# Kernel tuning notes

Measured on AMD Instinct MI355X. Metric: run time of the kernel, lower is better.

## Reference

```python
import jax, jax.numpy as jnp
import numpy as np

B, T, DIM = 1, 2048, 1024
NUM_HEADS, HEAD_DIM = 8, 128
ATTN_SCALE = 0.12


def _rms_norm(x):
    # F.rms_norm(x, x.size(-1)) with no weight; eps defaults to machine eps
    eps = jnp.asarray(jnp.finfo(x.dtype).eps, x.dtype)
    return x * jax.lax.rsqrt(jnp.mean(x * x, axis=-1, keepdims=True) + eps)


def _rotary_tables(seq_len, head_dim):
    # (1/1024) ** linspace(0,1,head_dim//4), then pad with head_dim//4 zeros
    freq = (1.0 / 1024.0) ** jnp.linspace(0.0, 1.0, head_dim // 4, dtype=jnp.float32)
    ang = jnp.concatenate([freq, jnp.zeros(head_dim // 4, jnp.float32)])  # [hd/2]
    theta = jnp.arange(seq_len, dtype=jnp.float32)[:, None] * ang[None, :]  # [T, hd/2]
    return jnp.cos(theta), jnp.sin(theta)


def _apply_rotary(x, cos, sin):
    # x: [B, T, H, hd]
    x1, x2 = jnp.split(x.astype(jnp.float32), 2, axis=-1)
    c = cos[None, :, None, :]
    s = sin[None, :, None, :]
    y1 = x1 * c + x2 * s
    y2 = -x1 * s + x2 * c
    return jnp.concatenate([y1, y2], axis=-1).astype(x.dtype)


def setup_inputs() -> dict:
    key = jax.random.key(0)
    ks = jax.random.split(key, 5)
    bound = (3.0 ** 0.5) * 0.5 * DIM ** (-0.5)
    x = jax.random.normal(ks[0], (B, T, DIM), jnp.float32)
    ve = jax.random.normal(ks[1], (B, T, NUM_HEADS * HEAD_DIM), jnp.float32)
    qkv_w = jax.random.uniform(ks[2], (3, NUM_HEADS * HEAD_DIM, DIM), jnp.float32, -bound, bound)
    lambdas = jnp.array([0.5, 0.5], jnp.float32)
    # original zero-inits c_proj; use small random weight so the output is nontrivial
    c_proj_w = jax.random.uniform(ks[3], (DIM, NUM_HEADS * HEAD_DIM), jnp.float32, -bound, bound)
    return {"x": x, "ve": ve, "qkv_w": qkv_w, "lambdas": lambdas, "c_proj_w": c_proj_w}


def reference(x, ve, qkv_w, lambdas, c_proj_w):
    Bx, Tx, D = x.shape
    H, hd = NUM_HEADS, HEAD_DIM
    # fused QKV projection: weight [3*H*hd, D]
    qkv = x @ qkv_w.reshape(3 * H * hd, D).T            # [B, T, 3*H*hd]
    qkv = qkv.reshape(Bx, Tx, 3 * H, hd)
    q, k, v = jnp.split(qkv, 3, axis=-2)                # each [B, T, H, hd]
    q, k = _rms_norm(q), _rms_norm(k)
    cos, sin = _rotary_tables(Tx, hd)
    q, k = _apply_rotary(q, cos, sin), _apply_rotary(k, cos, sin)
    v = lambdas[0] * v + lambdas[1] * ve.reshape(v.shape)
    att = jnp.einsum('bthd,bshd->bhts', q, k) * ATTN_SCALE
    causal = jnp.tril(jnp.ones((Tx, Tx), bool))
    att = jnp.where(causal[None, None], att, -jnp.inf)
    att = jax.nn.softmax(att, axis=-1)
    y = jnp.einsum('bhts,bshd->bthd', att, v).reshape(Bx, Tx, H * hd)
    return y @ c_proj_w.T
```

## Files before the change

### kernel.cpp

```cpp
#include <hip/hip_runtime.h>


typedef __attribute__((ext_vector_type(8))) short short8;
typedef __attribute__((ext_vector_type(4))) short short4b;
typedef __attribute__((ext_vector_type(4))) float fx4;
typedef __attribute__((ext_vector_type(8))) unsigned short ushort8;
typedef __attribute__((ext_vector_type(4))) unsigned short ushort4v;
typedef __attribute__((ext_vector_type(2))) unsigned short ushort2v;
typedef __attribute__((ext_vector_type(4))) float float4v;

#define T_SEQ 2048
#define NH 8
#define HD 128

__device__ __forceinline__ unsigned short f2bf(float f) {
  union { float f; unsigned u; } v; v.f = f;
  unsigned u = v.u;
  u += 0x7fffu + ((u >> 16) & 1u);
  return (unsigned short)(u >> 16);
}
__device__ __forceinline__ short bf_t(float f) {
  union { float f; unsigned u; } v; v.f = f;
  return (short)(v.u >> 16);
}
__device__ __forceinline__ float bf2f(unsigned short h) {
  union { unsigned u; float f; } v; v.u = ((unsigned)h) << 16;
  return v.f;
}

typedef __attribute__((address_space(1))) unsigned int glb_u32;
typedef __attribute__((address_space(3))) unsigned int lds_u32;
__device__ __forceinline__ void gl_lds16(const unsigned short* g, unsigned short* l) {
  __builtin_amdgcn_global_load_lds((const glb_u32*)g, (lds_u32*)l, 16, 0, 0);
}

__global__ __launch_bounds__(256) void cast3_kernel(
    const float* __restrict__ x, const float* __restrict__ w1,
    const float* __restrict__ w2, unsigned short* __restrict__ o) {
  long q = (long)blockIdx.x * 256 + threadIdx.x;
  const float* src;
  if (q < 524288)        src = x  + 4 * q;
  else if (q < 1310720)  src = w1 + 4 * (q - 524288);
  else                   src = w2 + 4 * (q - 1310720);
  float4v v = *(const float4v*)src;
  ushort4v r;
  r[0] = f2bf(v[0]); r[1] = f2bf(v[1]); r[2] = f2bf(v[2]); r[3] = f2bf(v[3]);
  *(ushort4v*)(o + 4 * q) = r;
}

template <bool OUT_BF16, int BM, int BN, int BK>
__global__ __launch_bounds__(256) void gemm_bt5(
    const unsigned short* __restrict__ A, const unsigned short* __restrict__ B,
    void* __restrict__ Cp, int M, int N, int K) {
  constexpr int MT = BM / 32;
  constexpr int NT = BN / 32;
  constexpr int KQ = BK / 32;
  constexpr int CPR = BK / 8;
  constexpr int ASEG = BM * BK / 512;
  constexpr int NLOAD = (BM + BN) * BK / 512 / 4;
  __shared__ unsigned short a_sh[2][BM * BK];
  __shared__ unsigned short b_sh[2][BN * BK];
  const int tid = threadIdx.x;
  const int wave = tid >> 6, lane = tid & 63;
  const int ln = lane & 15, quad = lane >> 4;
  const int wm = wave & 1, wn = wave >> 1;
  const long arow0 = (long)blockIdx.y * BM;
  const long brow0 = (long)blockIdx.x * BN;

  const unsigned short* gsrc[NLOAD];
  unsigned short* ldst[NLOAD];
  int bstr[NLOAD];
  for (int i = 0; i < NLOAD; ++i) {
    int s = wave * NLOAD + i;
    int isB = s >= ASEG;
    int srel = isB ? s - ASEG : s;
    int li = srel * 64 + lane;
    int row = li / CPR, posc = li % CPR;
    int c = posc ^ ((row >> 1) & (CPR - 1));
    gsrc[i] = (isB ? B + brow0 * (long)K : A + arow0 * (long)K)
              + (long)row * K + c * 8;
    ldst[i] = (isB ? &b_sh[0][0] : &a_sh[0][0]) + srel * 512;
    bstr[i] = (isB ? BN : BM) * BK;
  }
  for (int i = 0; i < NLOAD; ++i) gl_lds16(gsrc[i], ldst[i]);

  fx4 acc[MT][NT] = {};
  int cur = 0;
  for (int k0 = 0; k0 < K; k0 += BK, cur ^= 1) {
    __syncthreads();
    if (k0 + BK < K)
      for (int i = 0; i < NLOAD; ++i)
        gl_lds16(gsrc[i] + k0 + BK, ldst[i] + (cur ^ 1) * bstr[i]);
    const unsigned short* ash = &a_sh[cur][0];
    const unsigned short* bsh = &b_sh[cur][0];
    short8 af[KQ][MT], bfr[KQ][NT];
    for (int kq = 0; kq < KQ; ++kq) {
      for (int mt = 0; mt < MT; ++mt) {
        int m = wm * (BM / 2) + mt * 16 + ln;
        int pos = (kq * 4 + quad) ^ ((m >> 1) & (CPR - 1));
        af[kq][mt] = *(const short8*)&ash[m * BK + pos * 8];
      }
      for (int nt = 0; nt < NT; ++nt) {
        int n = wn * (BN / 2) + nt * 16 + ln;
        int pos = (kq * 4 + quad) ^ ((n >> 1) & (CPR - 1));
        bfr[kq][nt] = *(const short8*)&bsh[n * BK + pos * 8];
      }
    }
    for (int kq = 0; kq < KQ; ++kq)
      for (int mt = 0; mt < MT; ++mt)
        for (int nt = 0; nt < NT; ++nt)
          acc[mt][nt] = __builtin_amdgcn_mfma_f32_16x16x32_bf16(
              af[kq][mt], bfr[kq][nt], acc[mt][nt], 0, 0, 0);
  }
  for (int mt = 0; mt < MT; ++mt)
    for (int nt = 0; nt < NT; ++nt)
      for (int r = 0; r < 4; ++r) {
        long row = arow0 + wm * (BM / 2) + mt * 16 + quad * 4 + r;
        long col = brow0 + wn * (BN / 2) + nt * 16 + ln;
        float v = acc[mt][nt][r];
        if constexpr (OUT_BF16)
          ((unsigned short*)Cp)[row * N + col] = f2bf(v);
        else
          ((float*)Cp)[row * N + col] = v;
      }
}

__global__ __launch_bounds__(256) void qk_norm_rope2(
    const unsigned short* __restrict__ qkv, unsigned short* __restrict__ qh,
    unsigned short* __restrict__ kh) {
  const int idx = blockIdx.x * 4 + (threadIdx.x >> 6);
  const int lane = threadIdx.x & 63;
  const int which = idx & 1, h = (idx >> 1) & 7, t = idx >> 4;
  const unsigned short* src = qkv + (long)t * 3072 + which * 1024 + h * 128;
  float x1 = bf2f(src[lane]);
  float x2 = bf2f(src[64 + lane]);
  float ss = x1 * x1 + x2 * x2;
  for (int off = 1; off < 64; off <<= 1) ss += __shfl_xor(ss, off);
  float rn = rsqrtf(ss * (1.0f / 128.0f) + 1.1920929e-7f);
  float ang = (lane < 32) ? exp2f(-10.0f * (float)lane / 31.0f) : 0.0f;
  float th = (float)t * ang;
  float sv = __sinf(th), cv = __cosf(th);
  float y1 = ( x1 * cv + x2 * sv) * rn;
  float y2 = (-x1 * sv + x2 * cv) * rn;
  unsigned short* dst = (which ? kh : qh) + ((long)h * T_SEQ + t) * 128;
  dst[lane] = f2bf(y1);
  dst[64 + lane] = f2bf(y2);
}

__global__ __launch_bounds__(256) void v_combine_t(
    const unsigned short* __restrict__ qkv, const float* __restrict__ ve,
    const float* __restrict__ lambdas, unsigned short* __restrict__ vt) {
  __shared__ unsigned short lt[128 * 72];
  const int tt = blockIdx.x, h = blockIdx.y;
  const int tid = threadIdx.x;
  const float l0 = lambdas[0], l1 = lambdas[1];
  const int r = tid >> 2, cb = (tid & 3) * 32;
  const unsigned short* vs = qkv + (long)(tt * 64 + r) * 3072 + 2048 + h * 128 + cb;
  const float* es = ve + (long)(tt * 64 + r) * 1024 + h * 128 + cb;
  ushort8 vv[4];
  for (int q = 0; q < 4; ++q) vv[q] = *(const ushort8*)(vs + 8 * q);
  float4v ee[8];
  for (int q = 0; q < 8; ++q) ee[q] = *(const float4v*)(es + 4 * q);
  for (int j = 0; j < 32; ++j) {
    float v = bf2f(vv[j >> 3][j & 7]) * l0 + ee[j >> 2][j & 3] * l1;
    lt[(cb + j) * 72 + r] = f2bf(v);
  }
  __syncthreads();
  const int d = tid >> 1, half = tid & 1;
  unsigned short* dst = vt + ((long)h * HD + d) * T_SEQ + tt * 64 + half * 32;
  const unsigned short* srcl = &lt[d * 72];
  for (int g = 0; g < 8; ++g) {
    int p0 = half * 32 + g * 4;
    int kv0 = ((p0 >> 5) & 1) * 32 + ((p0 >> 2) & 1) * 16 + ((p0 >> 3) & 3) * 4;
    *(ushort4v*)(dst + g * 4) = *(const ushort4v*)(srcl + kv0);
  }
}

#define ATT_C1 0.17312340490667562f
#define ATT_C2 23.083120654223415f

__global__ __launch_bounds__(256, 2) void attn_part(
    const unsigned short* __restrict__ qh, const unsigned short* __restrict__ kh,
    const unsigned short* __restrict__ vt, unsigned short* __restrict__ Yp,
    float* __restrict__ lp) {
  __shared__ unsigned short kbuf[2][8192];
  __shared__ unsigned short vbuf[2][8192];
  const int tid = threadIdx.x;
  const int wave = tid >> 6, lane = tid & 63;
  const int ln = lane & 15, quad = lane >> 4;
  const int qt = blockIdx.x, h = blockIdx.y, ch = blockIdx.z;
  const int jmax = 2 * qt + 1;
  const int j0 = ch * 4;
  if (j0 > jmax) return;
  const int j1 = min(j0 + 3, jmax);

  int qg[2];
  short8 qf[2][4];
  for (int s = 0; s < 2; ++s) {
    qg[s] = qt * 128 + wave * 32 + s * 16 + ln;
    const unsigned short* qbase = qh + ((long)h * T_SEQ + qg[s]) * 128;
    for (int kc = 0; kc < 4; ++kc)
      qf[s][kc] = *(const short8*)(qbase + kc * 32 + quad * 8);
  }
  fx4 accy[2][8] = {};
  float l_loc[2] = {0.f, 0.f};

  const unsigned short* kg[4]; unsigned short* kl[4];
  const unsigned short* vg[4]; unsigned short* vl[4];
  for (int i = 0; i < 4; ++i) {
    int s = wave * 4 + i;
    { int li = s * 64 + lane; int row = li >> 4, posc = li & 15;
      int c = posc ^ (row & 15);
      kg[i] = kh + ((long)h * T_SEQ + row) * 128 + c * 8;
      kl[i] = &kbuf[0][s * 512]; }
    { int li = s * 64 + lane; int row = li >> 3, posc = li & 7;
      int c = posc ^ (row & 7);
      vg[i] = vt + ((long)h * HD + row) * T_SEQ + c * 8;
      vl[i] = &vbuf[0][s * 512]; }
  }
  for (int i = 0; i < 4; ++i) gl_lds16(kg[i] + (long)j0 * 8192, kl[i]);
  for (int i = 0; i < 4; ++i) gl_lds16(vg[i] + (long)j0 * 64, vl[i]);

  int cur = 0;
  for (int jt = j0; jt <= j1; ++jt, cur ^= 1) {
    __syncthreads();
    if (jt < j1) {
      int nb = (cur ^ 1) * 8192;
      for (int i = 0; i < 4; ++i) gl_lds16(kg[i] + (long)(jt + 1) * 8192, kl[i] + nb);
      for (int i = 0; i < 4; ++i) gl_lds16(vg[i] + (long)(jt + 1) * 64, vl[i] + nb);
    }
    const unsigned short* kb_ = &kbuf[cur][0];
    fx4 s4[2][4];
    for (int kt = 0; kt < 4; ++kt) {
      s4[0][kt] = fx4{0.f, 0.f, 0.f, 0.f};
      s4[1][kt] = fx4{0.f, 0.f, 0.f, 0.f};
      for (int kc = 0; kc < 4; ++kc) {
        int pos = (kc * 4 + quad) ^ ln;
        short8 kf = *(const short8*)&kb_[(kt * 16 + ln) * 128 + pos * 8];
        s4[0][kt] = __builtin_amdgcn_mfma_f32_16x16x32_bf16(kf, qf[0][kc], s4[0][kt], 0, 0, 0);
        s4[1][kt] = __builtin_amdgcn_mfma_f32_16x16x32_bf16(kf, qf[1][kc], s4[1][kt], 0, 0, 0);
      }
    }
    short4b pb[2][4];
    for (int s = 0; s < 2; ++s)
      for (int kt = 0; kt < 4; ++kt) {
        int kvb = jt * 64 + kt * 16 + quad * 4;
        float p[4];
        for (int r = 0; r < 4; ++r)
          p[r] = exp2f(fmaf(s4[s][kt][r], ATT_C1, -ATT_C2));
        if (jt * 64 + kt * 16 + 15 > qt * 128 + wave * 32 + s * 16) {
          for (int r = 0; r < 4; ++r) if (kvb + r > qg[s]) p[r] = 0.f;
        }
        l_loc[s] += (p[0] + p[1]) + (p[2] + p[3]);
        pb[s][kt] = short4b{ bf_t(p[0]), bf_t(p[1]), bf_t(p[2]), bf_t(p[3]) };
      }
    const unsigned short* vb_ = &vbuf[cur][0];
    for (int kh2 = 0; kh2 < 2; ++kh2) {
      for (int dt = 0; dt < 8; ++dt) {
        int row = dt * 16 + ln;
        int pos = (kh2 * 4 + quad) ^ (ln & 7);
        short8 va = *(const short8*)&vb_[row * 64 + pos * 8];
        short4b va0 = { va[0], va[1], va[2], va[3] };
        short4b va1 = { va[4], va[5], va[6], va[7] };
        for (int s = 0; s < 2; ++s) {
          accy[s][dt] = __builtin_amdgcn_mfma_f32_16x16x16bf16_1k(
              va0, pb[s][kh2 * 2], accy[s][dt], 0, 0, 0);
          accy[s][dt] = __builtin_amdgcn_mfma_f32_16x16x16bf16_1k(
              va1, pb[s][kh2 * 2 + 1], accy[s][dt], 0, 0, 0);
        }
      }
    }
  }

  int cbase = qt + ((qt - 1) * (qt - 1)) / 4;
  const long pp = (long)(h * 72 + cbase + ch);
  for (int s = 0; s < 2; ++s) {
    float l = l_loc[s];
    l += __shfl_xor(l, 16);
    l += __shfl_xor(l, 32);
    int q = wave * 32 + s * 16 + ln;
    if (quad == 0) lp[pp * 128 + q] = l;
    unsigned short* yb = Yp + pp * 16384 + (long)q * 128;
    for (int dt = 0; dt < 8; ++dt) {
      ushort4v o;
      for (int r = 0; r < 4; ++r) o[r] = f2bf(accy[s][dt][r]);
      *(ushort4v*)(yb + dt * 16 + quad * 4) = o;
    }
  }
}

__global__ __launch_bounds__(256) void attn_combine(
    const unsigned short* __restrict__ Yp, const float* __restrict__ lp,
    unsigned short* __restrict__ y) {
  const int bx = blockIdx.x, h = blockIdx.y;
  const int qt = bx >> 1, sub = bx & 1;
  const int tid = threadIdx.x;
  const int row = sub * 64 + (tid >> 2), cb = (tid & 3) * 32;
  const int nc = (qt >> 1) + 1;
  const int cbase = qt + ((qt - 1) * (qt - 1)) / 4;
  float acc[32];
  for (int j = 0; j < 32; ++j) acc[j] = 0.f;
  float ltot = 0.f;
  for (int c = 0; c < nc; ++c) {
    long pp = (long)(h * 72 + cbase + c);
    const unsigned short* ys = Yp + pp * 16384 + (long)row * 128 + cb;
    ltot += lp[pp * 128 + row];
    for (int q8 = 0; q8 < 4; ++q8) {
      ushort8 v = *(const ushort8*)(ys + q8 * 8);
      for (int j = 0; j < 8; ++j) acc[q8 * 8 + j] += bf2f(v[j]);
    }
  }
  float inv = 1.f / ltot;
  unsigned short* dst = y + (long)(qt * 128 + row) * 1024 + h * 128 + cb;
  for (int q8 = 0; q8 < 4; ++q8) {
    ushort8 o;
    for (int j = 0; j < 8; ++j) o[j] = f2bf(acc[q8 * 8 + j] * inv);
    *(ushort8*)(dst + q8 * 8) = o;
  }
}

extern "C" void kernel_launch(void* const* d_in, const int* in_sizes, int n_in,
                              void* d_out, int out_size, void* d_ws, size_t ws_size,
                              hipStream_t stream) {
  const float* x       = (const float*)d_in[0];
  const float* ve      = (const float*)d_in[1];
  const float* qkv_w   = (const float*)d_in[2];
  const float* lambdas = (const float*)d_in[3];
  const float* c_proj  = (const float*)d_in[4];
  char* ws = (char*)d_ws;
  unsigned short* qkv_bf = (unsigned short*)(ws);
  unsigned short* x_bf   = (unsigned short*)(ws + 12582912);
  unsigned short* wqkv   = (unsigned short*)(ws + 16777216);
  unsigned short* wproj  = (unsigned short*)(ws + 23068672);
  unsigned short* qhat   = (unsigned short*)(ws + 25165824);
  unsigned short* khat   = (unsigned short*)(ws + 29360128);
  unsigned short* vtb    = (unsigned short*)(ws + 33554432);
  unsigned short* ybf    = (unsigned short*)(ws + 37748736);
  unsigned short* Yp     = (unsigned short*)(ws);
  float*          lpart  = (float*)(ws + 18874368);
  float* out = (float*)d_out;

  cast3_kernel<<<6144, 256, 0, stream>>>(x, qkv_w, c_proj, x_bf);
  gemm_bt5<true, 128, 128, 32><<<dim3(24, 16), 256, 0, stream>>>(x_bf, wqkv, qkv_bf, 2048, 3072, 1024);
  qk_norm_rope2<<<8192, 256, 0, stream>>>(qkv_bf, qhat, khat);
  v_combine_t<<<dim3(32, 8), 256, 0, stream>>>(qkv_bf, ve, lambdas, vtb);
  attn_part<<<dim3(16, 8, 8), 256, 0, stream>>>(qhat, khat, vtb, Yp, lpart);
  attn_combine<<<dim3(32, 8), 256, 0, stream>>>(Yp, lpart, ybf);
  gemm_bt5<false, 64, 64, 64><<<dim3(16, 32), 256, 0, stream>>>(ybf, wproj, out, 2048, 1024, 1024);
}
```

Measured before the change: 198.3 us.

## Fuse QK RMS-norm, rotary and V combine/transpose into QKV GEMM epilogue

```diff
diff --git a/kernel.cpp b/kernel.cpp
--- a/kernel.cpp
+++ b/kernel.cpp
@@ -46,6 +46,147 @@
   ushort4v r;
   r[0] = f2bf(v[0]); r[1] = f2bf(v[1]); r[2] = f2bf(v[2]); r[3] = f2bf(v[3]);
   *(ushort4v*)(o + 4 * q) = r;
+}
+
+__global__ __launch_bounds__(256) void rope_tab(
+    float* __restrict__ rc, float* __restrict__ rs) {
+  int idx = blockIdx.x * 256 + threadIdx.x;
+  int t = idx >> 5, d = idx & 31;
+  float ang = exp2f(-10.0f * (float)d / 31.0f);
+  float th = (float)t * ang;
+  rc[idx] = __cosf(th);
+  rs[idx] = __sinf(th);
+}
+
+__global__ __launch_bounds__(256) void gemm1_fused(
+    const unsigned short* __restrict__ A, const unsigned short* __restrict__ B,
+    const float* __restrict__ ve, const float* __restrict__ lambdas,
+    const float* __restrict__ rc, const float* __restrict__ rs,
+    unsigned short* __restrict__ qh, unsigned short* __restrict__ kh,
+    unsigned short* __restrict__ vt) {
+  constexpr int K = 1024;
+  __shared__ unsigned short smem[2][12288];
+  const int tid = threadIdx.x;
+  const int wave = tid >> 6, lane = tid & 63;
+  const int ln = lane & 15, quad = lane >> 4;
+  const int wm = wave & 1, wn = wave >> 1;
+  const long arow0 = (long)blockIdx.y * 64;
+  const long brow0 = (long)blockIdx.x * 128;
+  const int which = blockIdx.x >> 3, h = blockIdx.x & 7;
+
+  const unsigned short* gsrc[6];
+  unsigned short* ldst[6];
+  for (int i = 0; i < 6; ++i) {
+    int s = wave * 6 + i;
+    int isB = s >= 8;
+    int srel = isB ? s - 8 : s;
+    int li = srel * 64 + lane;
+    int row = li >> 3, posc = li & 7;
+    int c = posc ^ ((row >> 1) & 7);
+    gsrc[i] = (isB ? B + brow0 * (long)K : A + arow0 * (long)K)
+              + (long)row * K + c * 8;
+    ldst[i] = &smem[0][(isB ? 4096 : 0) + srel * 512];
+  }
+  for (int i = 0; i < 6; ++i) gl_lds16(gsrc[i], ldst[i]);
+
+  fx4 acc[2][4] = {};
+  int cur = 0;
+  for (int k0 = 0; k0 < K; k0 += 64, cur ^= 1) {
+    __syncthreads();
+    if (k0 + 64 < K)
+      for (int i = 0; i < 6; ++i)
+        gl_lds16(gsrc[i] + k0 + 64, ldst[i] + (cur ^ 1) * 12288);
+    const unsigned short* ash = &smem[cur][0];
+    const unsigned short* bsh = &smem[cur][4096];
+    short8 af[2][2], bfr[2][4];
+    for (int kq = 0; kq < 2; ++kq) {
+      for (int mt = 0; mt < 2; ++mt) {
+        int m = wm * 32 + mt * 16 + ln;
+        int pos = (kq * 4 + quad) ^ ((m >> 1) & 7);
+        af[kq][mt] = *(const short8*)&ash[m * 64 + pos * 8];
+      }
+      for (int nt = 0; nt < 4; ++nt) {
+        int n = wn * 64 + nt * 16 + ln;
+        int pos = (kq * 4 + quad) ^ ((n >> 1) & 7);
+        bfr[kq][nt] = *(const short8*)&bsh[n * 64 + pos * 8];
+      }
+    }
+    for (int kq = 0; kq < 2; ++kq)
+      for (int mt = 0; mt < 2; ++mt)
+        for (int nt = 0; nt < 4; ++nt)
+          acc[mt][nt] = __builtin_amdgcn_mfma_f32_16x16x32_bf16(
+              af[kq][mt], bfr[kq][nt], acc[mt][nt], 0, 0, 0);
+  }
+
+  __syncthreads();
+  float* esh = (float*)&smem[0][0];
+  if (which == 2) {
+    const float l0 = lambdas[0], l1 = lambdas[1];
+    for (int mt = 0; mt < 2; ++mt)
+      for (int nt = 0; nt < 4; ++nt)
+        for (int r = 0; r < 4; ++r) {
+          int row = wm * 32 + mt * 16 + quad * 4 + r;
+          int col = wn * 64 + nt * 16 + ln;
+          float vev = ve[(arow0 + row) * 1024 + h * 128 + col];
+          esh[row * 132 + col] = l0 * acc[mt][nt][r] + l1 * vev;
+        }
+  } else {
+    for (int mt = 0; mt < 2; ++mt)
+      for (int nt = 0; nt < 4; ++nt)
+        for (int r = 0; r < 4; ++r) {
+          int row = wm * 32 + mt * 16 + quad * 4 + r;
+          int col = wn * 64 + nt * 16 + ln;
+          esh[row * 132 + col] = acc[mt][nt][r];
+        }
+  }
+  __syncthreads();
+
+  if (which < 2) {
+    const int lrow = tid >> 2, qq = tid & 3;
+    const long t = arow0 + lrow;
+    float4v x1[4], x2[4];
+    float ss = 0.f;
+    for (int i = 0; i < 4; ++i) {
+      x1[i] = *(const float4v*)&esh[lrow * 132 + qq * 16 + 4 * i];
+      x2[i] = *(const float4v*)&esh[lrow * 132 + 64 + qq * 16 + 4 * i];
+      ss += x1[i][0]*x1[i][0] + x1[i][1]*x1[i][1] + x1[i][2]*x1[i][2] + x1[i][3]*x1[i][3];
+      ss += x2[i][0]*x2[i][0] + x2[i][1]*x2[i][1] + x2[i][2]*x2[i][2] + x2[i][3]*x2[i][3];
+    }
+    ss += __shfl_xor(ss, 1);
+    ss += __shfl_xor(ss, 2);
+    float rn = rsqrtf(ss * (1.0f / 128.0f) + 1.1920929e-7f);
+    float4v cv[4], sv[4];
+    if (qq < 2) {
+      for (int i = 0; i < 4; ++i) {
+        cv[i] = *(const float4v*)&rc[t * 32 + qq * 16 + 4 * i];
+        sv[i] = *(const float4v*)&rs[t * 32 + qq * 16 + 4 * i];
+      }
+    } else {
+      for (int i = 0; i < 4; ++i) { cv[i] = float4v{1,1,1,1}; sv[i] = float4v{0,0,0,0}; }
+    }
+    ushort8 o1[2], o2[2];
+    for (int j = 0; j < 16; ++j) {
+      float a = x1[j >> 2][j & 3], b = x2[j >> 2][j & 3];
+      float c = cv[j >> 2][j & 3], s = sv[j >> 2][j & 3];
+      o1[j >> 3][j & 7] = f2bf(( a * c + b * s) * rn);
+      o2[j >> 3][j & 7] = f2bf((-a * s + b * c) * rn);
+    }
+    unsigned short* dst = (which ? kh : qh) + ((long)h * T_SEQ + t) * 128 + qq * 16;
+    *(ushort8*)(dst)      = o1[0];
+    *(ushort8*)(dst + 8)  = o1[1];
+    *(ushort8*)(dst + 64)     = o2[0];
+    *(ushort8*)(dst + 64 + 8) = o2[1];
+  } else {
+    const int d = tid >> 1, half = tid & 1;
+    unsigned short* dst = vt + ((long)h * HD + d) * T_SEQ + arow0 + half * 32;
+    for (int g = 0; g < 8; ++g) {
+      int p0 = half * 32 + g * 4;
+      int kv0 = ((p0 >> 5) & 1) * 32 + ((p0 >> 2) & 1) * 16 + ((p0 >> 3) & 3) * 4;
+      ushort4v o;
+      for (int j = 0; j < 4; ++j) o[j] = f2bf(esh[(kv0 + j) * 132 + d]);
+      *(ushort4v*)(dst + g * 4) = o;
+    }
+  }
 }
 
 template <bool OUT_BF16, int BM, int BN, int BK>
@@ -123,57 +264,6 @@
         else
           ((float*)Cp)[row * N + col] = v;
       }
-}
-
-__global__ __launch_bounds__(256) void qk_norm_rope2(
-    const unsigned short* __restrict__ qkv, unsigned short* __restrict__ qh,
-    unsigned short* __restrict__ kh) {
-  const int idx = blockIdx.x * 4 + (threadIdx.x >> 6);
-  const int lane = threadIdx.x & 63;
-  const int which = idx & 1, h = (idx >> 1) & 7, t = idx >> 4;
-  const unsigned short* src = qkv + (long)t * 3072 + which * 1024 + h * 128;
-  float x1 = bf2f(src[lane]);
-  float x2 = bf2f(src[64 + lane]);
-  float ss = x1 * x1 + x2 * x2;
-  for (int off = 1; off < 64; off <<= 1) ss += __shfl_xor(ss, off);
-  float rn = rsqrtf(ss * (1.0f / 128.0f) + 1.1920929e-7f);
-  float ang = (lane < 32) ? exp2f(-10.0f * (float)lane / 31.0f) : 0.0f;
-  float th = (float)t * ang;
-  float sv = __sinf(th), cv = __cosf(th);
-  float y1 = ( x1 * cv + x2 * sv) * rn;
-  float y2 = (-x1 * sv + x2 * cv) * rn;
-  unsigned short* dst = (which ? kh : qh) + ((long)h * T_SEQ + t) * 128;
-  dst[lane] = f2bf(y1);
-  dst[64 + lane] = f2bf(y2);
-}
-
-__global__ __launch_bounds__(256) void v_combine_t(
-    const unsigned short* __restrict__ qkv, const float* __restrict__ ve,
-    const float* __restrict__ lambdas, unsigned short* __restrict__ vt) {
-  __shared__ unsigned short lt[128 * 72];
-  const int tt = blockIdx.x, h = blockIdx.y;
-  const int tid = threadIdx.x;
-  const float l0 = lambdas[0], l1 = lambdas[1];
-  const int r = tid >> 2, cb = (tid & 3) * 32;
-  const unsigned short* vs = qkv + (long)(tt * 64 + r) * 3072 + 2048 + h * 128 + cb;
-  const float* es = ve + (long)(tt * 64 + r) * 1024 + h * 128 + cb;
-  ushort8 vv[4];
-  for (int q = 0; q < 4; ++q) vv[q] = *(const ushort8*)(vs + 8 * q);
-  float4v ee[8];
-  for (int q = 0; q < 8; ++q) ee[q] = *(const float4v*)(es + 4 * q);
-  for (int j = 0; j < 32; ++j) {
-    float v = bf2f(vv[j >> 3][j & 7]) * l0 + ee[j >> 2][j & 3] * l1;
-    lt[(cb + j) * 72 + r] = f2bf(v);
-  }
-  __syncthreads();
-  const int d = tid >> 1, half = tid & 1;
-  unsigned short* dst = vt + ((long)h * HD + d) * T_SEQ + tt * 64 + half * 32;
-  const unsigned short* srcl = &lt[d * 72];
-  for (int g = 0; g < 8; ++g) {
-    int p0 = half * 32 + g * 4;
-    int kv0 = ((p0 >> 5) & 1) * 32 + ((p0 >> 2) & 1) * 16 + ((p0 >> 3) & 3) * 4;
-    *(ushort4v*)(dst + g * 4) = *(const ushort4v*)(srcl + kv0);
-  }
 }
 
 #define ATT_C1 0.17312340490667562f
@@ -328,7 +418,6 @@
   const float* lambdas = (const float*)d_in[3];
   const float* c_proj  = (const float*)d_in[4];
   char* ws = (char*)d_ws;
-  unsigned short* qkv_bf = (unsigned short*)(ws);
   unsigned short* x_bf   = (unsigned short*)(ws + 12582912);
   unsigned short* wqkv   = (unsigned short*)(ws + 16777216);
   unsigned short* wproj  = (unsigned short*)(ws + 23068672);
@@ -338,12 +427,14 @@
   unsigned short* ybf    = (unsigned short*)(ws + 37748736);
   unsigned short* Yp     = (unsigned short*)(ws);
   float*          lpart  = (float*)(ws + 18874368);
+  float*          ropec  = (float*)(ws + 37748736);
+  float*          ropes  = (float*)(ws + 38010880);
   float* out = (float*)d_out;
 
   cast3_kernel<<<6144, 256, 0, stream>>>(x, qkv_w, c_proj, x_bf);
-  gemm_bt5<true, 128, 128, 32><<<dim3(24, 16), 256, 0, stream>>>(x_bf, wqkv, qkv_bf, 2048, 3072, 1024);
-  qk_norm_rope2<<<8192, 256, 0, stream>>>(qkv_bf, qhat, khat);
-  v_combine_t<<<dim3(32, 8), 256, 0, stream>>>(qkv_bf, ve, lambdas, vtb);
+  rope_tab<<<256, 256, 0, stream>>>(ropec, ropes);
+  gemm1_fused<<<dim3(24, 32), 256, 0, stream>>>(
+      x_bf, wqkv, ve, lambdas, ropec, ropes, qhat, khat, vtb);
   attn_part<<<dim3(16, 8, 8), 256, 0, stream>>>(qhat, khat, vtb, Yp, lpart);
   attn_combine<<<dim3(32, 8), 256, 0, stream>>>(Yp, lpart, ybf);
   gemm_bt5<false, 64, 64, 64><<<dim3(16, 32), 256, 0, stream>>>(ybf, wproj, out, 2048, 1024, 1024);
```

After: 224.7 us. 1.13x slower.
